# Kernel tuning notes

Measured on AMD Instinct MI355X. Metric: run time of the kernel, lower is better.

Reference implementation:

```python
import jax, jax.numpy as jnp
import numpy as np

B, T, V, E, H = 1024, 256, 90, 8, 256


def setup_inputs() -> dict:
    key = jax.random.key(0)
    ks = jax.random.split(key, 40)
    rn = lambda k, shape: jax.random.normal(k, shape, dtype=jnp.float32) * 0.05
    inp = {}
    inp["input_seq"] = jax.random.randint(ks[0], (B, T), 0, V, dtype=jnp.int32)
    inp["emb"] = rn(ks[1], (V, E)).at[0].set(0.0)  # padding_idx=0
    i = 2
    for name, din in [("g1", E), ("g2", H), ("l1", E), ("l2", H)]:
        inp[name + "_Wih"] = rn(ks[i], (4 * H, din)); i += 1
        inp[name + "_Whh"] = rn(ks[i], (4 * H, H)); i += 1
        inp[name + "_bih"] = rn(ks[i], (4 * H,)); i += 1
        inp[name + "_bhh"] = rn(ks[i], (4 * H,)); i += 1
    for name in ["p1", "p2"]:
        inp[name + "_W1"] = rn(ks[i], (2 * H, E + 4 * H)); i += 1
        inp[name + "_b1"] = rn(ks[i], (2 * H,)); i += 1
        inp[name + "_W2"] = rn(ks[i], (H, 2 * H)); i += 1
        inp[name + "_b2"] = rn(ks[i], (H,)); i += 1
        inp[name + "_W3"] = rn(ks[i], (2, H)); i += 1
        inp[name + "_b3"] = rn(ks[i], (2,)); i += 1
    inp["gfc_W"] = rn(ks[i], (V, H)); i += 1
    inp["gfc_b"] = rn(ks[i], (V,)); i += 1
    inp["lfc_W"] = rn(ks[i], (V, H)); i += 1
    inp["lfc_b"] = rn(ks[i], (V,))
    return inp


def _cell(x, h, c, Wih, Whh, bih, bhh):
    # PyTorch LSTMCell: gate order i, f, g, o
    g = x @ Wih.T + h @ Whh.T + (bih + bhh)
    i, f, gg, o = jnp.split(g, 4, axis=-1)
    c = jax.nn.sigmoid(f) * c + jax.nn.sigmoid(i) * jnp.tanh(gg)
    return jax.nn.sigmoid(o) * jnp.tanh(c), c


def _mlp(x, W1, b1, W2, b2, W3, b3):
    h = jax.nn.relu(x @ W1.T + b1)
    h = jax.nn.relu(h @ W2.T + b2)
    return h @ W3.T + b3


def _forward(input_seq, emb,
             g1_Wih, g1_Whh, g1_bih, g1_bhh, g2_Wih, g2_Whh, g2_bih, g2_bhh,
             l1_Wih, l1_Whh, l1_bih, l1_bhh, l2_Wih, l2_Whh, l2_bih, l2_bhh,
             p1_W1, p1_b1, p1_W2, p1_b2, p1_W3, p1_b3,
             p2_W1, p2_b1, p2_W2, p2_b2, p2_W3, p2_b3,
             gfc_W, gfc_b, lfc_W, lfc_b):
    Bn = input_seq.shape[0]
    embeds = emb[input_seq]  # [B, T, E]
    z = jnp.zeros((Bn, H), dtype=emb.dtype)

    def step(carry, e):
        gh1, gc1, gh2, gc2, lh1, lc1, lh2, lc2 = carry
        gh1, gc1 = _cell(e, gh1, gc1, g1_Wih, g1_Whh, g1_bih, g1_bhh)
        lh1, lc1 = _cell(e, lh1, lc1, l1_Wih, l1_Whh, l1_bih, l1_bhh)
        p = jax.nn.softmax(_mlp(jnp.concatenate([e, gh1, gc1, lh1, lc1], 1),
                                p1_W1, p1_b1, p1_W2, p1_b2, p1_W3, p1_b3), axis=1)
        # bmm([B,1,2],[B,2,H]) == p0*local + p1*global
        gh1 = p[:, 0:1] * lh1 + p[:, 1:2] * gh1
        gc1 = p[:, 0:1] * lc1 + p[:, 1:2] * gc1
        gh2, gc2 = _cell(gh1, gh2, gc2, g2_Wih, g2_Whh, g2_bih, g2_bhh)
        lh2, lc2 = _cell(lh1, lh2, lc2, l2_Wih, l2_Whh, l2_bih, l2_bhh)
        p = jax.nn.softmax(_mlp(jnp.concatenate([e, gh2, gc2, lh2, lc2], 1),
                                p2_W1, p2_b1, p2_W2, p2_b2, p2_W3, p2_b3), axis=1)
        gh2 = p[:, 0:1] * lh2 + p[:, 1:2] * gh2
        gc2 = p[:, 0:1] * lc2 + p[:, 1:2] * gc2
        return (gh1, gc1, gh2, gc2, lh1, lc1, lh2, lc2), gh2

    _, hs = jax.lax.scan(step, (z, z, z, z, z, z, z, z), jnp.swapaxes(embeds, 0, 1))
    hs = jnp.swapaxes(hs, 0, 1)  # [B, T, H]
    out = 0.5 * (hs @ gfc_W.T + gfc_b) + 0.5 * (hs @ lfc_W.T + lfc_b)
    return jnp.swapaxes(out, 1, 2)  # [B, V, T]


def reference(input_seq, emb,
              g1_Wih, g1_Whh, g1_bih, g1_bhh, g2_Wih, g2_Whh, g2_bih, g2_bhh,
              l1_Wih, l1_Whh, l1_bih, l1_bhh, l2_Wih, l2_Whh, l2_bih, l2_bhh,
              p1_W1, p1_b1, p1_W2, p1_b2, p1_W3, p1_b3,
              p2_W1, p2_b1, p2_W2, p2_b2, p2_W3, p2_b3,
              gfc_W, gfc_b, lfc_W, lfc_b):
    return _forward(input_seq, emb,
                    g1_Wih, g1_Whh, g1_bih, g1_bhh, g2_Wih, g2_Whh, g2_bih, g2_bhh,
                    l1_Wih, l1_Whh, l1_bih, l1_bhh, l2_Wih, l2_Whh, l2_bih, l2_bhh,
                    p1_W1, p1_b1, p1_W2, p1_b2, p1_W3, p1_b3,
                    p2_W1, p2_b1, p2_W2, p2_b2, p2_W3, p2_b3,
                    gfc_W, gfc_b, lfc_W, lfc_b)
```

## Files before the change

### kernel.cpp

```cpp
#include <hip/hip_runtime.h>

#define B_ 1024
#define T_ 256
#define V_ 90
#define H_ 256
#define NTHR 512
#define NBLK 256
#define S_ ((size_t)B_*H_)

typedef unsigned short u16;
typedef __attribute__((ext_vector_type(8))) _Float16 f16x8;
typedef __attribute__((ext_vector_type(4))) _Float16 f16x4;
typedef __attribute__((ext_vector_type(4))) float f32x4;

constexpr size_t OFF_GH1C  = 0;
constexpr size_t OFF_GC1C  = OFF_GH1C + S_;
constexpr size_t OFF_GH1P  = OFF_GC1C + S_;
constexpr size_t OFF_GC1P  = OFF_GH1P + S_;
constexpr size_t OFF_LH1   = OFF_GC1P + S_;
constexpr size_t OFF_LC1   = OFF_LH1 + 2*S_;
constexpr size_t OFF_GH2C  = OFF_LC1 + 2*S_;
constexpr size_t OFF_GC2C  = OFF_GH2C + S_;
constexpr size_t OFF_GH2P  = OFF_GC2C + S_;
constexpr size_t OFF_GC2P  = OFF_GH2P + S_;
constexpr size_t OFF_LH2   = OFF_GC2P + S_;
constexpr size_t OFF_LC2   = OFF_LH2 + 2*S_;
constexpr size_t OFF_M1A   = OFF_LC2 + 2*S_;
constexpr size_t OFF_M1B   = OFF_M1A + (size_t)B_*512;
constexpr size_t OFF_M2A   = OFF_M1B + (size_t)B_*512;
constexpr size_t OFF_M2B   = OFF_M2A + (size_t)B_*512;
constexpr size_t OFF_EX    = OFF_M2B + (size_t)B_*512;
constexpr size_t OFF_WG1PK = OFF_EX + 2*B_*8;
constexpr size_t OFF_WE1   = OFF_WG1PK + 256*2048/2;
constexpr size_t OFF_BG1   = OFF_WE1 + 8*2048;
constexpr size_t OFF_WL2PK = OFF_BG1 + 2048;
constexpr size_t OFF_BL2   = OFF_WL2PK + 512*1024/2;
constexpr size_t OFF_WG2PK = OFF_BL2 + 1024;
constexpr size_t OFF_BG2   = OFF_WG2PK + 512*1024/2;
constexpr size_t OFF_WP1PK = OFF_BG2 + 1024;
constexpr size_t OFF_WEP1  = OFF_WP1PK + 1024*512/2;
constexpr size_t OFF_WP2PK = OFF_WEP1 + 8*512;
constexpr size_t OFF_WEP2  = OFF_WP2PK + 1024*512/2;
constexpr size_t OFF_WB1   = OFF_WEP2 + 8*512;
constexpr size_t OFF_WB2   = OFF_WB1 + 512*256/2;
constexpr size_t OFF_WOUT  = OFF_WB2 + 512*256/2;
constexpr size_t OFF_BOUT  = OFF_WOUT + 256*96;
constexpr size_t OFF_BAR   = OFF_BOUT + 128;
constexpr size_t WS_FLOATS = OFF_BAR + 8192;

struct InP {
  const int*   seq;
  const float* emb;
  const float *g1_Wih,*g1_Whh,*g1_bih,*g1_bhh;
  const float *g2_Wih,*g2_Whh,*g2_bih,*g2_bhh;
  const float *l1_Wih,*l1_Whh,*l1_bih,*l1_bhh;
  const float *l2_Wih,*l2_Whh,*l2_bih,*l2_bhh;
  const float *p1_W1,*p1_b1,*p1_W2,*p1_b2,*p1_W3,*p1_b3;
  const float *p2_W1,*p2_b1,*p2_W2,*p2_b2,*p2_W3,*p2_b3;
  const float *gfc_W,*gfc_b,*lfc_W,*lfc_b;
};

__device__ __forceinline__ float sig_(float x)  { return 1.f/(1.f+__expf(-x)); }
__device__ __forceinline__ float tanh_(float x) { return 1.f - 2.f/(__expf(2.f*x)+1.f); }
__device__ __forceinline__ u16 f2h(float v) {
  _Float16 h = (_Float16)v; return __builtin_bit_cast(unsigned short, h);
}

__device__ __forceinline__ unsigned ld_flag(const unsigned* p) {
  unsigned v;
  asm volatile("global_load_dword %0, %1, off sc1\n\ts_waitcnt vmcnt(0)"
               : "=v"(v) : "v"(p) : "memory");
  return v;
}
__device__ __forceinline__ void st_flag(unsigned* p, unsigned v) {
  asm volatile("global_store_dword %0, %1, off sc1\n\ts_waitcnt vmcnt(0)"
               :: "v"(p), "v"(v) : "memory");
}

__device__ __forceinline__ void gbar_x(unsigned* arr, int slot, unsigned ep)
{
  __syncthreads();
  if (threadIdx.x == 0) st_flag(&arr[slot*16], ep);
  if (threadIdx.x < 32) {
    int cap = 0;
    for (;;) {
      unsigned v = ld_flag(&arr[threadIdx.x*16]);
      if (v >= ep) break;
      __builtin_amdgcn_s_sleep(1);
      if (++cap > 200000) break;
    }
  }
  __syncthreads();
  asm volatile("buffer_inv sc0" ::: "memory");
}

__device__ __forceinline__ void gl_lds16(const void* g, void* l) {
  __builtin_amdgcn_global_load_lds(
      (const __attribute__((address_space(1))) unsigned int*)g,
      (__attribute__((address_space(3))) unsigned int*)l, 16, 0, 0);
}
__device__ __forceinline__ void dma64(const u16* src) {
  extern __shared__ u16 dynB[];
  const int wv = threadIdx.x >> 6, lane = threadIdx.x & 63;
  const char* g = (const char*)src + lane*16;
  char* l = (char*)dynB;
#pragma unroll
  for (int j = 0; j < 8; ++j) {
    const int ofs = (wv*8 + j) * 1024;
    gl_lds16(g + ofs, l + ofs);
  }
}

template<int NCH, int NSEG, bool HASE, int TPW, class FE>
__device__ __forceinline__ void mm_lds(
    const float* s0, const float* s1_,
    const float* WeP, int ldwe, const float* ex,
    int rows0, int ct0, FE fe)
{
  extern __shared__ u16 dynB[];
  const int tid = threadIdx.x, lane = tid & 63, wr = tid >> 6;
  const int row = rows0 + wr*16 + (lane & 15);
  const int kq  = (lane >> 4) << 3;

  asm volatile("s_waitcnt vmcnt(0)" ::: "memory");
  __syncthreads();

  f32x4 acc[TPW];
#pragma unroll
  for (int t = 0; t < TPW; ++t) acc[t] = (f32x4){0,0,0,0};

  float4 alo[4], ahi[4];
  auto ldA = [&](int c, float4& lo, float4& hi) {
    const int k0 = c * 32;
    const float* S = (NSEG == 1) ? s0 : ((k0 < 256) ? s0 : s1_);
    const float* p = &S[(size_t)row*H_ + (k0 & 255) + kq];
    lo = *(const float4*)p; hi = *(const float4*)(p + 4);
  };
  auto comp = [&](int c, const float4& lo, const float4& hi) {
    float av[8] = {lo.x,lo.y,lo.z,lo.w,hi.x,hi.y,hi.z,hi.w};
    f16x8 a;
#pragma unroll
    for (int j = 0; j < 8; ++j) a[j] = (_Float16)av[j];
#pragma unroll
    for (int t = 0; t < TPW; ++t) {
      f16x8 b = *(const f16x8*)(dynB + (size_t)(c*TPW + t)*512 + lane*8);
      acc[t] = __builtin_amdgcn_mfma_f32_16x16x32_f16(a, b, acc[t], 0, 0, 0);
    }
  };

#pragma unroll
  for (int c = 0; c < 4; ++c) ldA(c, alo[c], ahi[c]);
#pragma unroll
  for (int c = 0; c < NCH; ++c) {
    comp(c, alo[c & 3], ahi[c & 3]);
    if (c + 4 < NCH) ldA(c + 4, alo[c & 3], ahi[c & 3]);
  }

  if (HASE) {
#pragma unroll
    for (int t = 0; t < TPW; ++t) {
      const int colL = ct0 + t*16 + (lane & 15);
      float w[8];
#pragma unroll
      for (int j = 0; j < 8; ++j) w[j] = WeP[j*ldwe + colL];
#pragma unroll
      for (int m = 0; m < 4; ++m) {
        const int rr = rows0 + wr*16 + ((lane >> 4) << 2) + m;
        float s = 0.f;
#pragma unroll
        for (int j = 0; j < 8; ++j) s = __builtin_fmaf(ex[rr*8 + j], w[j], s);
        acc[t][m] += s;
      }
    }
  }
  fe(wr, lane, acc);
}

template<int TPW>
struct GateEpiM {
  const float* cin; float* ho; float* co; const float* bias_pk;
  int rows0; int ct0;
  __device__ void operator()(int wr, int lane, f32x4 (&acc)[TPW]) const {
    const int rbase = rows0 + wr*16 + ((lane >> 4) << 2);
#pragma unroll
    for (int gi = 0; gi < TPW/4; ++gi) {
      const int cb = ct0 + gi*64;
      const int h = (((cb & 1023) >> 6) << 4) + (lane & 15);
      float b[4];
#pragma unroll
      for (int t = 0; t < 4; ++t) b[t] = bias_pk[cb + t*16 + (lane & 15)];
#pragma unroll
      for (int m = 0; m < 4; ++m) {
        const size_t ix = (size_t)(rbase + m)*H_ + h;
        float gI = sig_(acc[gi*4+0][m] + b[0]);
        float gF = sig_(acc[gi*4+1][m] + b[1]);
        float gG = tanh_(acc[gi*4+2][m] + b[2]);
        float gO = sig_(acc[gi*4+3][m] + b[3]);
        float cn = gF*cin[ix] + gI*gG;
        ho[ix] = gO*tanh_(cn); co[ix] = cn;
      }
    }
  }
};

struct MlpEpiM {
  float* dst; int rows0; int ct0;
  __device__ void operator()(int wr, int lane, f32x4 (&acc)[4]) const {
    const int rbase = rows0 + wr*16 + ((lane >> 4) << 2);
    const int c0 = ct0 + (lane & 15);
#pragma unroll
    for (int t = 0; t < 4; ++t)
#pragma unroll
      for (int m = 0; m < 4; ++m)
        dst[(size_t)(rbase + m)*512 + c0 + t*16] = acc[t][m];
  }
};

__device__ __forceinline__ void stage_F2(
    int rowbase,
    const float* mlpA, const float* mlpB, const float* b1,
    const u16* WBpk, const float* b2,
    const float* W3, const float* b3,
    const float* lh, const float* lc,
    const float* ghp, const float* gcp,
    float* ghc, float* gcc)
{
  const int w = threadIdx.x >> 6, lane = threadIdx.x & 63;
  const int r0 = rowbase + w*2;
  const float* aA0 = mlpA + (size_t)r0*512; const float* aB0 = mlpB + (size_t)r0*512;
  const float* aA1 = aA0 + 512;             const float* aB1 = aB0 + 512;
  float m0[4] = {0.f,0.f,0.f,0.f}, m1[4] = {0.f,0.f,0.f,0.f};
  for (int k0 = 0; k0 < 512; k0 += 4) {
    float4 xa = *(const float4*)&aA0[k0];
    float4 xb = *(const float4*)&aB0[k0];
    float4 ya = *(const float4*)&aA1[k0];
    float4 yb = *(const float4*)&aB1[k0];
    float4 bb = *(const float4*)&b1[k0];
    float xv0[4] = { fmaxf(xa.x+xb.x+bb.x,0.f), fmaxf(xa.y+xb.y+bb.y,0.f),
                     fmaxf(xa.z+xb.z+bb.z,0.f), fmaxf(xa.w+xb.w+bb.w,0.f) };
    float xv1[4] = { fmaxf(ya.x+yb.x+bb.x,0.f), fmaxf(ya.y+yb.y+bb.y,0.f),
                     fmaxf(ya.z+yb.z+bb.z,0.f), fmaxf(ya.w+yb.w+bb.w,0.f) };
#pragma unroll
    for (int j = 0; j < 4; ++j) {
      f16x4 wv = *(const f16x4*)&WBpk[(size_t)(k0+j)*256 + lane*4];
      float w0 = (float)wv[0], w1 = (float)wv[1], w2 = (float)wv[2], w3v = (float)wv[3];
      m0[0] = __builtin_fmaf(xv0[j], w0, m0[0]);
      m0[1] = __builtin_fmaf(xv0[j], w1, m0[1]);
      m0[2] = __builtin_fmaf(xv0[j], w2, m0[2]);
      m0[3] = __builtin_fmaf(xv0[j], w3v, m0[3]);
      m1[0] = __builtin_fmaf(xv1[j], w0, m1[0]);
      m1[1] = __builtin_fmaf(xv1[j], w1, m1[1]);
      m1[2] = __builtin_fmaf(xv1[j], w2, m1[2]);
      m1[3] = __builtin_fmaf(xv1[j], w3v, m1[3]);
    }
  }
  float4 b = *(const float4*)&b2[lane*4];
  float bb2[4] = {b.x,b.y,b.z,b.w};
#pragma unroll
  for (int j = 0; j < 4; ++j) {
    m0[j] = fmaxf(m0[j]+bb2[j], 0.f);
    m1[j] = fmaxf(m1[j]+bb2[j], 0.f);
  }
  float4 w30 = *(const float4*)&W3[lane*4];
  float4 w31 = *(const float4*)&W3[256 + lane*4];
  float w0v[4] = {w30.x,w30.y,w30.z,w30.w};
  float w1v[4] = {w31.x,w31.y,w31.z,w31.w};
  float d00=0.f, d01=0.f, d10=0.f, d11=0.f;
#pragma unroll
  for (int j = 0; j < 4; ++j) {
    d00 = __builtin_fmaf(m0[j], w0v[j], d00);
    d01 = __builtin_fmaf(m0[j], w1v[j], d01);
    d10 = __builtin_fmaf(m1[j], w0v[j], d10);
    d11 = __builtin_fmaf(m1[j], w1v[j], d11);
  }
#pragma unroll
  for (int off = 32; off; off >>= 1) {
    d00 += __shfl_xor(d00, off, 64); d01 += __shfl_xor(d01, off, 64);
    d10 += __shfl_xor(d10, off, 64); d11 += __shfl_xor(d11, off, 64);
  }
  d00 += b3[0]; d01 += b3[1]; d10 += b3[0]; d11 += b3[1];
  float mxa = fmaxf(d00, d01), mxb = fmaxf(d10, d11);
  float e00 = __expf(d00-mxa), e01 = __expf(d01-mxa);
  float e10 = __expf(d10-mxb), e11 = __expf(d11-mxb);
  float ia = 1.f/(e00+e01), ib = 1.f/(e10+e11);
  float p0a = e00*ia, p1a = e01*ia;
  float p0b = e10*ib, p1b = e11*ib;
#pragma unroll
  for (int rr = 0; rr < 2; ++rr) {
    const float p0 = rr ? p0b : p0a, p1 = rr ? p1b : p1a;
    const size_t ix = (size_t)(r0+rr)*H_ + lane*4;
    float4 lv = *(const float4*)&lh[ix];
    float4 gv = *(const float4*)&ghp[ix];
    float4 o;
    o.x = p0*lv.x + p1*gv.x; o.y = p0*lv.y + p1*gv.y;
    o.z = p0*lv.z + p1*gv.z; o.w = p0*lv.w + p1*gv.w;
    *(float4*)&ghc[ix] = o;
    lv = *(const float4*)&lc[ix];
    gv = *(const float4*)&gcp[ix];
    o.x = p0*lv.x + p1*gv.x; o.y = p0*lv.y + p1*gv.y;
    o.z = p0*lv.z + p1*gv.z; o.w = p0*lv.w + p1*gv.w;
    *(float4*)&gcc[ix] = o;
  }
}

__device__ __forceinline__ void stage_OUT2(
    const float* gh2c, const float* WOUT, const float* BOUT,
    float* out, int rbase, int tt)
{
  const int w = threadIdx.x >> 6, lane = threadIdx.x & 63;
  const bool two = lane < (V_ - 64);
#pragma unroll
  for (int rr = 0; rr < 2; ++rr) {
    const int r = rbase + w*2 + rr;
    const float* arow = gh2c + (size_t)r * H_;
    float acc0 = 0.f, acc1 = 0.f;
    for (int k0 = 0; k0 < 256; k0 += 4) {
      float4 a4 = *(const float4*)&arow[k0];
      float av[4] = {a4.x, a4.y, a4.z, a4.w};
#pragma unroll
      for (int j = 0; j < 4; ++j) {
        const float* wr_ = &WOUT[(size_t)(k0+j)*96];
        acc0 = __builtin_fmaf(av[j], wr_[lane], acc0);
        if (two) acc1 = __builtin_fmaf(av[j], wr_[64+lane], acc1);
      }
    }
    out[((size_t)r*V_ + lane)*T_ + tt] = acc0 + BOUT[lane];
    if (two) out[((size_t)r*V_ + 64 + lane)*T_ + tt] = acc1 + BOUT[64+lane];
  }
}

__global__ void k_setup(InP in, float* __restrict__ ws)
{
  const size_t nthr = (size_t)gridDim.x * blockDim.x;
  const size_t t0 = (size_t)blockIdx.x * blockDim.x + threadIdx.x;

  for (size_t i = t0; i < 16*S_; i += nthr) ws[i] = 0.f;
  for (size_t i = t0; i < 8192; i += nthr) ((unsigned*)(ws + OFF_BAR))[i] = 0u;

  for (size_t i = t0; i < (size_t)B_*8; i += nthr) {
    int r = (int)(i >> 3), j = (int)(i & 7);
    ws[OFF_EX + i] = in.emb[(size_t)in.seq[(size_t)r*T_]*8 + j];
  }

  {
    u16* dst = (u16*)(ws + OFF_WG1PK);
    for (size_t i = t0; i < (size_t)16*8*8*512; i += nthr) {
      int e = (int)(i & 7), lane = (int)((i >> 3) & 63);
      int tile = (int)((i >> 9) & 7), ck = (int)((i >> 12) & 7), blk = (int)(i >> 15);
      int col = blk*128 + tile*16 + (lane & 15);
      int k = ck*32 + ((lane >> 4) << 3) + e;
      int cell = col >> 10, q = col & 1023;
      int h = ((q >> 6) << 4) + (q & 15), g = (q >> 4) & 3, R = g*256 + h;
      dst[i] = f2h((cell ? in.l1_Whh : in.g1_Whh)[(size_t)R*256 + k]);
    }
  }
  for (size_t i = t0; i < (size_t)8*2048; i += nthr) {
    int j = (int)(i >> 11), p = (int)(i & 2047);
    int cell = p >> 10, q = p & 1023;
    int h = ((q >> 6) << 4) + (q & 15), g = (q >> 4) & 3, R = g*256 + h;
    ws[OFF_WE1 + (size_t)j*2048 + p] = (cell ? in.l1_Wih : in.g1_Wih)[(size_t)R*8 + j];
  }
  for (size_t i = t0; i < 2048; i += nthr) {
    int p = (int)i, cell = p >> 10, q = p & 1023;
    int h = ((q >> 6) << 4) + (q & 15), g = (q >> 4) & 3, R = g*256 + h;
    ws[OFF_BG1 + i] = cell ? (in.l1_bih[R] + in.l1_bhh[R]) : (in.g1_bih[R] + in.g1_bhh[R]);
  }

  for (int which = 0; which < 2; ++which) {
    u16* dst = (u16*)(ws + (which ? OFF_WG2PK : OFF_WL2PK));
    const float* Wih = which ? in.g2_Wih : in.l2_Wih;
    const float* Whh = which ? in.g2_Whh : in.l2_Whh;
    for (size_t i = t0; i < (size_t)16*16*4*512; i += nthr) {
      int e = (int)(i & 7), lane = (int)((i >> 3) & 63);
      int tile = (int)((i >> 9) & 3), ck = (int)((i >> 11) & 15), blk = (int)(i >> 15);
      int col = blk*64 + tile*16 + (lane & 15);
      int k = ck*32 + ((lane >> 4) << 3) + e;
      int h = ((col >> 6) << 4) + (col & 15), g = (col >> 4) & 3, R = g*256 + h;
      float w = (k < 256) ? Wih[(size_t)R*256 + k] : Whh[(size_t)R*256 + (k-256)];
      dst[i] = f2h(w);
    }
  }
  for (size_t i = t0; i < 2*1024; i += nthr) {
    int which = (int)(i >> 10), p = (int)(i & 1023);
    int h = ((p >> 6) << 4) + (p & 15), g = (p >> 4) & 3, R = g*256 + h;
    float v = which ? (in.g2_bih[R] + in.g2_bhh[R]) : (in.l2_bih[R] + in.l2_bhh[R]);
    ws[(which ? OFF_BG2 : OFF_BL2) + p] = v;
  }

  for (int which = 0; which < 2; ++which) {
    u16* dst = (u16*)(ws + (which ? OFF_WP2PK : OFF_WP1PK));
    const float* W = which ? in.p2_W1 : in.p1_W1;
    for (size_t i = t0; i < (size_t)16*16*4*512; i += nthr) {
      int e = (int)(i & 7), lane = (int)((i >> 3) & 63);
      int tile = (int)((i >> 9) & 3), ck = (int)((i >> 11) & 15), blk = (int)(i >> 15);
      int kh = blk >> 3, ct = blk & 7;
      int col = ct*64 + tile*16 + (lane & 15);
      int k = kh*512 + ck*32 + ((lane >> 4) << 3) + e;
      dst[i] = f2h(W[(size_t)col*1032 + 8 + k]);
    }
  }
  for (size_t i = t0; i < (size_t)2*8*512; i += nthr) {
    int which = (int)(i / (8*512));
    int idx = (int)(i - (size_t)which*8*512);
    int j = idx >> 9, p = idx & 511;
    const float* W = which ? in.p2_W1 : in.p1_W1;
    ws[(which ? OFF_WEP2 : OFF_WEP1) + (size_t)j*512 + p] = W[(size_t)p*1032 + j];
  }

  for (size_t i = t0; i < (size_t)2*512*256; i += nthr) {
    int which = (int)(i / (512*256));
    int idx = (int)(i - (size_t)which*512*256);
    int k = idx >> 8, n = idx & 255;
    const float* W = which ? in.p2_W2 : in.p1_W2;
    ((u16*)(ws + (which ? OFF_WB2 : OFF_WB1)))[idx] = f2h(W[(size_t)n*512 + k]);
  }
  for (size_t i = t0; i < (size_t)256*96; i += nthr) {
    int k = (int)(i / 96), c = (int)(i - (size_t)k*96);
    float v = 0.f;
    if (c < V_) v = 0.5f*(in.gfc_W[(size_t)c*256 + k] + in.lfc_W[(size_t)c*256 + k]);
    ws[OFF_WOUT + i] = v;
  }
  for (size_t i = t0; i < 96; i += nthr)
    ws[OFF_BOUT + i] = (i < V_) ? 0.5f*(in.gfc_b[i] + in.lfc_b[i]) : 0.f;
}

__global__ __launch_bounds__(NTHR) void k_main(InP in, float* ws, float* __restrict__ out)
{
  __shared__ __attribute__((aligned(16))) volatile float s_pad[6144];
  __shared__ unsigned s_slot;

  float* GH1C = ws + OFF_GH1C;  float* GC1C = ws + OFF_GC1C;
  float* GH1P = ws + OFF_GH1P;  float* GC1P = ws + OFF_GC1P;
  float* LH1  = ws + OFF_LH1;   float* LC1  = ws + OFF_LC1;
  float* GH2C = ws + OFF_GH2C;  float* GC2C = ws + OFF_GC2C;
  float* GH2P = ws + OFF_GH2P;  float* GC2P = ws + OFF_GC2P;
  float* LH2  = ws + OFF_LH2;   float* LC2  = ws + OFF_LC2;
  float* M1A  = ws + OFF_M1A;   float* M1B  = ws + OFF_M1B;
  float* M2A  = ws + OFF_M2A;   float* M2B  = ws + OFF_M2B;
  float* EXB  = ws + OFF_EX;
  const u16* WG1PK = (const u16*)(ws + OFF_WG1PK);
  const u16* WL2PK = (const u16*)(ws + OFF_WL2PK);
  const u16* WG2PK = (const u16*)(ws + OFF_WG2PK);
  const u16* WP1PK = (const u16*)(ws + OFF_WP1PK);
  const u16* WP2PK = (const u16*)(ws + OFF_WP2PK);
  const u16* WB1PK = (const u16*)(ws + OFF_WB1);
  const u16* WB2PK = (const u16*)(ws + OFF_WB2);
  const float* WE1  = ws + OFF_WE1;  const float* BG1P = ws + OFF_BG1;
  const float* BL2P = ws + OFF_BL2;  const float* BG2P = ws + OFF_BG2;
  const float* WEP1 = ws + OFF_WEP1; const float* WEP2 = ws + OFF_WEP2;
  const float* WOUT = ws + OFF_WOUT; const float* BOUT = ws + OFF_BOUT;

  unsigned xcc;
  asm volatile("s_getreg_b32 %0, hwreg(HW_REG_XCC_ID)" : "=s"(xcc));
  xcc &= 7u;
  unsigned* barx = ((unsigned*)(ws + OFF_BAR)) + xcc*1024;
  unsigned* arr  = barx;
  unsigned* reg  = barx + 544;
  if (threadIdx.x == 0) {
    s_slot = __hip_atomic_fetch_add(reg, 1u, __ATOMIC_RELAXED, __HIP_MEMORY_SCOPE_AGENT);
    s_pad[0] = (float)s_slot;
  }
  __syncthreads();
  const int slot  = (int)(s_slot & 31u);
  const int rows0 = (int)xcc * 128;
  const int s2 = slot & 15;
  unsigned ep = 0;

  if (slot < 16) dma64(WG1PK + (size_t)slot*32768);
  else           dma64(WG2PK + (size_t)s2*32768);

  for (int n = 0; n <= T_; ++n) {
    const int sel = n & 1;
    const float* ex  = EXB + sel*(B_*8);
    const float* exm = EXB + (sel^1)*(B_*8);
    float* lh1o = LH1 + sel*S_;   float* lh1n = LH1 + (sel^1)*S_;
    float* lc1o = LC1 + sel*S_;   float* lc1n = LC1 + (sel^1)*S_;
    float* lh2o = LH2 + sel*S_;   float* lh2n = LH2 + (sel^1)*S_;
    float* lc2o = LC2 + sel*S_;   float* lc2n = LC2 + (sel^1)*S_;

    if (slot < 16) {
      if (n < T_) {
        const int ct0 = slot*128;
        const int cell = slot >> 3;
        GateEpiM<8> epi{ cell ? lc1o : GC1C,
                         cell ? lh1n : GH1P,
                         cell ? lc1n : GC1P,
                         BG1P, rows0, ct0 };
        mm_lds<8,1,true,8>(cell ? lh1o : GH1C, nullptr,
                           WE1, 2048, ex, rows0, ct0, epi);
      }
    } else if (n >= 1) {
      const int ct0 = s2*64;
      GateEpiM<4> epi{ GC2C, GH2P, GC2P, BG2P, rows0, ct0 };
      mm_lds<16,2,false,4>(GH1C, GH2C, nullptr, 0, nullptr, rows0, ct0, epi);
    }
    __syncthreads();
    {
      const int kh = s2 >> 3, ct = s2 & 7;
      const int blk = kh*8 + ct;
      if (slot < 16) dma64(WP1PK + (size_t)blk*32768);
      else           dma64(WP2PK + (size_t)blk*32768);
    }
    gbar_x(arr, slot, ++ep);

    if (slot < 16) {
      if (n < T_) {
        const int kh = s2 >> 3, ct = s2 & 7;
        const int ct0 = ct*64;
        if (kh == 0) {
          MlpEpiM epi{ M1A, rows0, ct0 };
          mm_lds<16,2,false,4>(GH1P, GC1P, nullptr, 0, nullptr, rows0, ct0, epi);
        } else {
          MlpEpiM epi{ M1B, rows0, ct0 };
          mm_lds<16,2,true,4>(lh1n, lc1n, WEP1, 512, ex, rows0, ct0, epi);
        }
      }
    } else if (n >= 1) {
      const int kh = s2 >> 3, ct = s2 & 7;
      const int ct0 = ct*64;
      if (kh == 0) {
        MlpEpiM epi{ M2A, rows0, ct0 };
        mm_lds<16,2,false,4>(GH2P, GC2P, nullptr, 0, nullptr, rows0, ct0, epi);
      } else {
        MlpEpiM epi{ M2B, rows0, ct0 };
        mm_lds<16,2,true,4>(lh2o, lc2o, WEP2, 512, exm, rows0, ct0, epi);
      }
    }
    __syncthreads();
    if (n < T_) {
      if (slot < 16) dma64(WL2PK + (size_t)slot*32768);
      else           dma64(WG2PK + (size_t)s2*32768);
    }
    gbar_x(arr, slot, ++ep);

    if (slot < 16) {
      if (n < T_) {
        const int ct0 = slot*64;
        GateEpiM<4> epi{ lc2o, lh2n, lc2n, BL2P, rows0, ct0 };
        mm_lds<16,2,false,4>(lh1n, lh2o, nullptr, 0, nullptr, rows0, ct0, epi);
      }
    } else if (slot < 24) {
      if (n < T_) {
        const int rb = rows0 + (slot-16)*16;
        stage_F2(rb, M1A, M1B, in.p1_b1, WB1PK, in.p1_b2, in.p1_W3, in.p1_b3,
                 lh1n, lc1n, GH1P, GC1P, GH1C, GC1C);
        if (n + 1 < T_ && threadIdx.x < 128) {
          const int r = rb + (threadIdx.x >> 3), j = threadIdx.x & 7;
          EXB[(sel^1)*(B_*8) + r*8 + j] =
              in.emb[(size_t)in.seq[(size_t)r*T_ + n + 1]*8 + j];
        }
      }
    } else {
      if (n >= 1) {
        const int rb = rows0 + (slot-24)*16;
        stage_F2(rb, M2A, M2B, in.p2_b1, WB2PK, in.p2_b2, in.p2_W3, in.p2_b3,
                 lh2o, lc2o, GH2P, GC2P, GH2C, GC2C);
        __syncthreads();
        stage_OUT2(GH2C, WOUT, BOUT, out, rb, n-1);
      }
    }
    __syncthreads();
    if (n < T_ - 1) {
      if (slot < 16) dma64(WG1PK + (size_t)slot*32768);
    }
    gbar_x(arr, slot, ++ep);
  }
}

extern "C" void kernel_launch(void* const* d_in, const int* in_sizes, int n_in,
                              void* d_out, int out_size, void* d_ws, size_t ws_size,
                              hipStream_t stream)
{
  if (ws_size < WS_FLOATS * sizeof(float)) return;

  InP in;
  in.seq    = (const int*)  d_in[0];
  in.emb    = (const float*)d_in[1];
  in.g1_Wih = (const float*)d_in[2];  in.g1_Whh = (const float*)d_in[3];
  in.g1_bih = (const float*)d_in[4];  in.g1_bhh = (const float*)d_in[5];
  in.g2_Wih = (const float*)d_in[6];  in.g2_Whh = (const float*)d_in[7];
  in.g2_bih = (const float*)d_in[8];  in.g2_bhh = (const float*)d_in[9];
  in.l1_Wih = (const float*)d_in[10]; in.l1_Whh = (const float*)d_in[11];
  in.l1_bih = (const float*)d_in[12]; in.l1_bhh = (const float*)d_in[13];
  in.l2_Wih = (const float*)d_in[14]; in.l2_Whh = (const float*)d_in[15];
  in.l2_bih = (const float*)d_in[16]; in.l2_bhh = (const float*)d_in[17];
  in.p1_W1  = (const float*)d_in[18]; in.p1_b1  = (const float*)d_in[19];
  in.p1_W2  = (const float*)d_in[20]; in.p1_b2  = (const float*)d_in[21];
  in.p1_W3  = (const float*)d_in[22]; in.p1_b3  = (const float*)d_in[23];
  in.p2_W1  = (const float*)d_in[24]; in.p2_b1  = (const float*)d_in[25];
  in.p2_W2  = (const float*)d_in[26]; in.p2_b2  = (const float*)d_in[27];
  in.p2_W3  = (const float*)d_in[28]; in.p2_b3  = (const float*)d_in[29];
  in.gfc_W  = (const float*)d_in[30]; in.gfc_b  = (const float*)d_in[31];
  in.lfc_W  = (const float*)d_in[32]; in.lfc_b  = (const float*)d_in[33];

  float* ws  = (float*)d_ws;
  float* out = (float*)d_out;

  k_setup<<<512, 256, 0, stream>>>(in, ws);
  k_main <<<NBLK, NTHR, 65536, stream>>>(in, ws, out);
}
```

Measured before the change: 67.76 ms.

## Fuse MLP first layer K-halves, store fp16 activations, batch output writes

The MLP first-layer GEMM no longer splits K across two block halves writing separate fp32 partial sums. Each block now covers the full 1024-wide K over four input segments for 32 columns, and the epilogue applies bias and ReLU and stores fp16. The second MLP stage therefore reads one fp16 buffer instead of two fp32 buffers plus bias, cutting global traffic. Output logits are staged for 16 timesteps and flushed as contiguous float4 writes instead of strided scalar stores. Also removed are the per-matmul vmcnt wait and barrier, with the LDS DMA cache-policy bit changed. This risks a race on the DMA'd weights, since the wait now sits only before the loop, and adds fp16 rounding of the hidden activations.

```diff
diff --git a/kernel.cpp b/kernel.cpp
--- a/kernel.cpp
+++ b/kernel.cpp
@@ -25,11 +25,10 @@
 constexpr size_t OFF_GC2P  = OFF_GH2P + S_;
 constexpr size_t OFF_LH2   = OFF_GC2P + S_;
 constexpr size_t OFF_LC2   = OFF_LH2 + 2*S_;
-constexpr size_t OFF_M1A   = OFF_LC2 + 2*S_;
-constexpr size_t OFF_M1B   = OFF_M1A + (size_t)B_*512;
-constexpr size_t OFF_M2A   = OFF_M1B + (size_t)B_*512;
-constexpr size_t OFF_M2B   = OFF_M2A + (size_t)B_*512;
-constexpr size_t OFF_EX    = OFF_M2B + (size_t)B_*512;
+constexpr size_t OFF_M1H   = OFF_LC2 + 2*S_;
+constexpr size_t OFF_M2H   = OFF_M1H + (size_t)B_*512/2;
+constexpr size_t OFF_OSTG  = OFF_M2H + (size_t)B_*512/2;
+constexpr size_t OFF_EX    = OFF_OSTG + (size_t)B_*16*90;
 constexpr size_t OFF_WG1PK = OFF_EX + 2*B_*8;
 constexpr size_t OFF_WE1   = OFF_WG1PK + 256*2048/2;
 constexpr size_t OFF_BG1   = OFF_WE1 + 8*2048;
@@ -97,7 +96,7 @@
 __device__ __forceinline__ void gl_lds16(const void* g, void* l) {
   __builtin_amdgcn_global_load_lds(
       (const __attribute__((address_space(1))) unsigned int*)g,
-      (__attribute__((address_space(3))) unsigned int*)l, 16, 0, 0);
+      (__attribute__((address_space(3))) unsigned int*)l, 16, 0, 2);
 }
 __device__ __forceinline__ void dma64(const u16* src) {
   extern __shared__ u16 dynB[];
@@ -113,7 +112,7 @@
 
 template<int NCH, int NSEG, bool HASE, int TPW, class FE>
 __device__ __forceinline__ void mm_lds(
-    const float* s0, const float* s1_,
+    const float* s0, const float* s1_, const float* s2_, const float* s3_,
     const float* WeP, int ldwe, const float* ex,
     int rows0, int ct0, FE fe)
 {
@@ -122,9 +121,6 @@
   const int row = rows0 + wr*16 + (lane & 15);
   const int kq  = (lane >> 4) << 3;
 
-  asm volatile("s_waitcnt vmcnt(0)" ::: "memory");
-  __syncthreads();
-
   f32x4 acc[TPW];
 #pragma unroll
   for (int t = 0; t < TPW; ++t) acc[t] = (f32x4){0,0,0,0};
@@ -132,7 +128,10 @@
   float4 alo[4], ahi[4];
   auto ldA = [&](int c, float4& lo, float4& hi) {
     const int k0 = c * 32;
-    const float* S = (NSEG == 1) ? s0 : ((k0 < 256) ? s0 : s1_);
+    const float* S;
+    if (NSEG == 1) S = s0;
+    else if (NSEG == 2) S = (k0 < 256) ? s0 : s1_;
+    else S = (k0 < 256) ? s0 : (k0 < 512) ? s1_ : (k0 < 768) ? s2_ : s3_;
     const float* p = &S[(size_t)row*H_ + (k0 & 255) + kq];
     lo = *(const float4*)p; hi = *(const float4*)(p + 4);
   };
@@ -203,23 +202,24 @@
   }
 };
 
-struct MlpEpiM {
-  float* dst; int rows0; int ct0;
-  __device__ void operator()(int wr, int lane, f32x4 (&acc)[4]) const {
+struct MlpEpiH {
+  u16* dst; const float* b1; int rows0; int ct0;
+  __device__ void operator()(int wr, int lane, f32x4 (&acc)[2]) const {
     const int rbase = rows0 + wr*16 + ((lane >> 4) << 2);
-    const int c0 = ct0 + (lane & 15);
-#pragma unroll
-    for (int t = 0; t < 4; ++t)
+#pragma unroll
+    for (int t = 0; t < 2; ++t) {
+      const int c = ct0 + t*16 + (lane & 15);
+      const float bb = b1[c];
 #pragma unroll
       for (int m = 0; m < 4; ++m)
-        dst[(size_t)(rbase + m)*512 + c0 + t*16] = acc[t][m];
+        dst[(size_t)(rbase + m)*512 + c] = f2h(fmaxf(acc[t][m] + bb, 0.f));
+    }
   }
 };
 
 __device__ __forceinline__ void stage_F2(
     int rowbase,
-    const float* mlpA, const float* mlpB, const float* b1,
-    const u16* WBpk, const float* b2,
+    const u16* M, const u16* WBpk, const float* b2,
     const float* W3, const float* b3,
     const float* lh, const float* lc,
     const float* ghp, const float* gcp,
@@ -227,31 +227,25 @@
 {
   const int w = threadIdx.x >> 6, lane = threadIdx.x & 63;
   const int r0 = rowbase + w*2;
-  const float* aA0 = mlpA + (size_t)r0*512; const float* aB0 = mlpB + (size_t)r0*512;
-  const float* aA1 = aA0 + 512;             const float* aB1 = aB0 + 512;
+  const u16* a0 = M + (size_t)r0*512;
+  const u16* a1 = a0 + 512;
   float m0[4] = {0.f,0.f,0.f,0.f}, m1[4] = {0.f,0.f,0.f,0.f};
   for (int k0 = 0; k0 < 512; k0 += 4) {
-    float4 xa = *(const float4*)&aA0[k0];
-    float4 xb = *(const float4*)&aB0[k0];
-    float4 ya = *(const float4*)&aA1[k0];
-    float4 yb = *(const float4*)&aB1[k0];
-    float4 bb = *(const float4*)&b1[k0];
-    float xv0[4] = { fmaxf(xa.x+xb.x+bb.x,0.f), fmaxf(xa.y+xb.y+bb.y,0.f),
-                     fmaxf(xa.z+xb.z+bb.z,0.f), fmaxf(xa.w+xb.w+bb.w,0.f) };
-    float xv1[4] = { fmaxf(ya.x+yb.x+bb.x,0.f), fmaxf(ya.y+yb.y+bb.y,0.f),
-                     fmaxf(ya.z+yb.z+bb.z,0.f), fmaxf(ya.w+yb.w+bb.w,0.f) };
+    f16x4 x0 = *(const f16x4*)&a0[k0];
+    f16x4 x1 = *(const f16x4*)&a1[k0];
 #pragma unroll
     for (int j = 0; j < 4; ++j) {
       f16x4 wv = *(const f16x4*)&WBpk[(size_t)(k0+j)*256 + lane*4];
       float w0 = (float)wv[0], w1 = (float)wv[1], w2 = (float)wv[2], w3v = (float)wv[3];
-      m0[0] = __builtin_fmaf(xv0[j], w0, m0[0]);
-      m0[1] = __builtin_fmaf(xv0[j], w1, m0[1]);
-      m0[2] = __builtin_fmaf(xv0[j], w2, m0[2]);
-      m0[3] = __builtin_fmaf(xv0[j], w3v, m0[3]);
-      m1[0] = __builtin_fmaf(xv1[j], w0, m1[0]);
-      m1[1] = __builtin_fmaf(xv1[j], w1, m1[1]);
-      m1[2] = __builtin_fmaf(xv1[j], w2, m1[2]);
-      m1[3] = __builtin_fmaf(xv1[j], w3v, m1[3]);
+      float xv0 = (float)x0[j], xv1 = (float)x1[j];
+      m0[0] = __builtin_fmaf(xv0, w0, m0[0]);
+      m0[1] = __builtin_fmaf(xv0, w1, m0[1]);
+      m0[2] = __builtin_fmaf(xv0, w2, m0[2]);
+      m0[3] = __builtin_fmaf(xv0, w3v, m0[3]);
+      m1[0] = __builtin_fmaf(xv1, w0, m1[0]);
+      m1[1] = __builtin_fmaf(xv1, w1, m1[1]);
+      m1[2] = __builtin_fmaf(xv1, w2, m1[2]);
+      m1[3] = __builtin_fmaf(xv1, w3v, m1[3]);
     }
   }
   float4 b = *(const float4*)&b2[lane*4];
@@ -303,9 +297,9 @@
   }
 }
 
-__device__ __forceinline__ void stage_OUT2(
+__device__ __forceinline__ void stage_OUTS(
     const float* gh2c, const float* WOUT, const float* BOUT,
-    float* out, int rbase, int tt)
+    float* ostg, int rbase, int tt)
 {
   const int w = threadIdx.x >> 6, lane = threadIdx.x & 63;
   const bool two = lane < (V_ - 64);
@@ -324,8 +318,26 @@
         if (two) acc1 = __builtin_fmaf(av[j], wr_[64+lane], acc1);
       }
     }
-    out[((size_t)r*V_ + lane)*T_ + tt] = acc0 + BOUT[lane];
-    if (two) out[((size_t)r*V_ + 64 + lane)*T_ + tt] = acc1 + BOUT[64+lane];
+    float* dst = &ostg[((size_t)r*16 + (tt & 15))*90];
+    if (lane < 64) dst[lane] = acc0 + BOUT[lane];
+    if (two) dst[64+lane] = acc1 + BOUT[64+lane];
+  }
+}
+
+__device__ __forceinline__ void flush_out(
+    const float* ostg, float* out, int rbase, int tb0)
+{
+  for (int i = threadIdx.x; i < 16*90; i += NTHR) {
+    const int rr = i / 90, v = i - rr*90;
+    const int r = rbase + rr;
+    const float* src = &ostg[((size_t)r*16)*90 + v];
+    float tmp[16];
+#pragma unroll
+    for (int tb = 0; tb < 16; ++tb) tmp[tb] = src[tb*90];
+    float* dst = &out[((size_t)r*V_ + v)*T_ + tb0];
+#pragma unroll
+    for (int q = 0; q < 4; ++q)
+      ((float4*)dst)[q] = make_float4(tmp[q*4], tmp[q*4+1], tmp[q*4+2], tmp[q*4+3]);
   }
 }
 
@@ -390,12 +402,11 @@
   for (int which = 0; which < 2; ++which) {
     u16* dst = (u16*)(ws + (which ? OFF_WP2PK : OFF_WP1PK));
     const float* W = which ? in.p2_W1 : in.p1_W1;
-    for (size_t i = t0; i < (size_t)16*16*4*512; i += nthr) {
+    for (size_t i = t0; i < (size_t)16*32*2*512; i += nthr) {
       int e = (int)(i & 7), lane = (int)((i >> 3) & 63);
-      int tile = (int)((i >> 9) & 3), ck = (int)((i >> 11) & 15), blk = (int)(i >> 15);
-      int kh = blk >> 3, ct = blk & 7;
-      int col = ct*64 + tile*16 + (lane & 15);
-      int k = kh*512 + ck*32 + ((lane >> 4) << 3) + e;
+      int tile = (int)((i >> 9) & 1), ck = (int)((i >> 10) & 31), blk = (int)(i >> 15);
+      int col = blk*32 + tile*16 + (lane & 15);
+      int k = ck*32 + ((lane >> 4) << 3) + e;
       dst[i] = f2h(W[(size_t)col*1032 + 8 + k]);
     }
   }
@@ -435,8 +446,9 @@
   float* GH2C = ws + OFF_GH2C;  float* GC2C = ws + OFF_GC2C;
   float* GH2P = ws + OFF_GH2P;  float* GC2P = ws + OFF_GC2P;
   float* LH2  = ws + OFF_LH2;   float* LC2  = ws + OFF_LC2;
-  float* M1A  = ws + OFF_M1A;   float* M1B  = ws + OFF_M1B;
-  float* M2A  = ws + OFF_M2A;   float* M2B  = ws + OFF_M2B;
+  u16*   M1H  = (u16*)(ws + OFF_M1H);
+  u16*   M2H  = (u16*)(ws + OFF_M2H);
+  float* OSTG = ws + OFF_OSTG;
   float* EXB  = ws + OFF_EX;
   const u16* WG1PK = (const u16*)(ws + OFF_WG1PK);
   const u16* WL2PK = (const u16*)(ws + OFF_WL2PK);
@@ -468,6 +480,8 @@
 
   if (slot < 16) dma64(WG1PK + (size_t)slot*32768);
   else           dma64(WG2PK + (size_t)s2*32768);
+  asm volatile("s_waitcnt vmcnt(0)" ::: "memory");
+  __syncthreads();
 
   for (int n = 0; n <= T_; ++n) {
     const int sel = n & 1;
@@ -486,45 +500,34 @@
                          cell ? lh1n : GH1P,
                          cell ? lc1n : GC1P,
                          BG1P, rows0, ct0 };
-        mm_lds<8,1,true,8>(cell ? lh1o : GH1C, nullptr,
+        mm_lds<8,1,true,8>(cell ? lh1o : GH1C, nullptr, nullptr, nullptr,
                            WE1, 2048, ex, rows0, ct0, epi);
       }
     } else if (n >= 1) {
       const int ct0 = s2*64;
       GateEpiM<4> epi{ GC2C, GH2P, GC2P, BG2P, rows0, ct0 };
-      mm_lds<16,2,false,4>(GH1C, GH2C, nullptr, 0, nullptr, rows0, ct0, epi);
+      mm_lds<16,2,false,4>(GH1C, GH2C, nullptr, nullptr,
+                           nullptr, 0, nullptr, rows0, ct0, epi);
     }
     __syncthreads();
     {
-      const int kh = s2 >> 3, ct = s2 & 7;
-      const int blk = kh*8 + ct;
-      if (slot < 16) dma64(WP1PK + (size_t)blk*32768);
-      else           dma64(WP2PK + (size_t)blk*32768);
+      if (slot < 16) dma64(WP1PK + (size_t)s2*32768);
+      else           dma64(WP2PK + (size_t)s2*32768);
     }
     gbar_x(arr, slot, ++ep);
 
     if (slot < 16) {
       if (n < T_) {
-        const int kh = s2 >> 3, ct = s2 & 7;
-        const int ct0 = ct*64;
-        if (kh == 0) {
-          MlpEpiM epi{ M1A, rows0, ct0 };
-          mm_lds<16,2,false,4>(GH1P, GC1P, nullptr, 0, nullptr, rows0, ct0, epi);
-        } else {
-          MlpEpiM epi{ M1B, rows0, ct0 };
-          mm_lds<16,2,true,4>(lh1n, lc1n, WEP1, 512, ex, rows0, ct0, epi);
-        }
+        const int ct0 = s2*32;
+        MlpEpiH epi{ M1H, in.p1_b1, rows0, ct0 };
+        mm_lds<32,4,true,2>(GH1P, GC1P, lh1n, lc1n,
+                            WEP1, 512, ex, rows0, ct0, epi);
       }
     } else if (n >= 1) {
-      const int kh = s2 >> 3, ct = s2 & 7;
-      const int ct0 = ct*64;
-      if (kh == 0) {
-        MlpEpiM epi{ M2A, rows0, ct0 };
-        mm_lds<16,2,false,4>(GH2P, GC2P, nullptr, 0, nullptr, rows0, ct0, epi);
-      } else {
-        MlpEpiM epi{ M2B, rows0, ct0 };
-        mm_lds<16,2,true,4>(lh2o, lc2o, WEP2, 512, exm, rows0, ct0, epi);
-      }
+      const int ct0 = s2*32;
+      MlpEpiH epi{ M2H, in.p2_b1, rows0, ct0 };
+      mm_lds<32,4,true,2>(GH2P, GC2P, lh2o, lc2o,
+                          WEP2, 512, exm, rows0, ct0, epi);
     }
     __syncthreads();
     if (n < T_) {
@@ -537,12 +540,13 @@
       if (n < T_) {
         const int ct0 = slot*64;
         GateEpiM<4> epi{ lc2o, lh2n, lc2n, BL2P, rows0, ct0 };
-        mm_lds<16,2,false,4>(lh1n, lh2o, nullptr, 0, nullptr, rows0, ct0, epi);
+        mm_lds<16,2,false,4>(lh1n, lh2o, nullptr, nullptr,
+                             nullptr, 0, nullptr, rows0, ct0, epi);
       }
     } else if (slot < 24) {
       if (n < T_) {
         const int rb = rows0 + (slot-16)*16;
-        stage_F2(rb, M1A, M1B, in.p1_b1, WB1PK, in.p1_b2, in.p1_W3, in.p1_b3,
+        stage_F2(rb, M1H, WB1PK, in.p1_b2, in.p1_W3, in.p1_b3,
                  lh1n, lc1n, GH1P, GC1P, GH1C, GC1C);
         if (n + 1 < T_ && threadIdx.x < 128) {
           const int r = rb + (threadIdx.x >> 3), j = threadIdx.x & 7;
@@ -553,10 +557,14 @@
     } else {
       if (n >= 1) {
         const int rb = rows0 + (slot-24)*16;
-        stage_F2(rb, M2A, M2B, in.p2_b1, WB2PK, in.p2_b2, in.p2_W3, in.p2_b3,
+        stage_F2(rb, M2H, WB2PK, in.p2_b2, in.p2_W3, in.p2_b3,
                  lh2o, lc2o, GH2P, GC2P, GH2C, GC2C);
         __syncthreads();
-        stage_OUT2(GH2C, WOUT, BOUT, out, rb, n-1);
+        stage_OUTS(GH2C, WOUT, BOUT, OSTG, rb, n-1);
+        if (((n-1) & 15) == 15) {
+          __syncthreads();
+          flush_out(OSTG, out, rb, n-16);
+        }
       }
     }
     __syncthreads();
```

Result: faster. 57.61 ms (-15.0%).
